# Performance work log

Hardware: AMD Instinct MI355X
Metric: run time of the kernel (lower is better)

## Reference

```python
import jax, jax.numpy as jnp
import numpy as np

N, E, G, H, F_IN = 100_000, 3_200_000, 256, 16, 7
RRELU_SLOPE = (1.0 / 8.0 + 1.0 / 3.0) / 2.0  # eval-mode RReLU uses mean slope


def rrelu(x):
    return jnp.where(x >= 0, x, RRELU_SLOPE * x)


def gcn_conv(x, edge_index, edge_weight, W, b, n_nodes):
    """PyG GCNConv: add self-loops, symmetric norm, gather-matmul-scatter."""
    row, col = edge_index[0], edge_index[1]
    loop = jnp.arange(n_nodes)
    row = jnp.concatenate([row, loop])
    col = jnp.concatenate([col, loop])
    w = jnp.concatenate([edge_weight, jnp.ones((n_nodes,), x.dtype)])
    deg = jax.ops.segment_sum(w, col, num_segments=n_nodes)
    dis = jnp.where(deg > 0, jax.lax.rsqrt(jnp.maximum(deg, 1e-12)), 0.0)
    norm = dis[row] * w * dis[col]            # [E+N]
    h = x @ W                                  # [N, out]
    msg = h[row] * norm[:, None]               # gather + scale
    return jax.ops.segment_sum(msg, col, num_segments=n_nodes) + b


def max_pool_neighbor_x(x, edge_index, n_nodes):
    row, col = edge_index[0], edge_index[1]
    loop = jnp.arange(n_nodes)
    row = jnp.concatenate([row, loop])
    col = jnp.concatenate([col, loop])
    return jax.ops.segment_max(x[row], col, num_segments=n_nodes)


def setup_inputs() -> dict:
    key = jax.random.key(0)
    ks = jax.random.split(key, 12)
    x = jax.random.normal(ks[0], (N, F_IN), jnp.float32)
    edge_index = jax.random.randint(ks[1], (2, E), 0, N)
    edge_weights = jax.random.uniform(ks[2], (E,), jnp.float32)
    batch = (jnp.arange(N) * G) // N  # sorted, every graph non-empty
    s = 0.2
    W1 = jax.random.normal(ks[3], (F_IN, H), jnp.float32) * s
    b1 = jnp.zeros((H,), jnp.float32)
    W2 = jax.random.normal(ks[4], (H, H), jnp.float32) * s
    b2 = jnp.zeros((H,), jnp.float32)
    Wl1 = jax.random.normal(ks[5], (H, H), jnp.float32) * s
    bl1 = jax.random.normal(ks[6], (H,), jnp.float32) * s
    Wl3 = jax.random.normal(ks[7], (H, H), jnp.float32) * s
    bl3 = jax.random.normal(ks[8], (H,), jnp.float32) * s
    Wl4 = jax.random.normal(ks[9], (H, 1), jnp.float32) * s
    bl4 = jax.random.normal(ks[10], (1,), jnp.float32) * s
    return {"x": x, "edge_index": edge_index, "batch": batch,
            "edge_weights": edge_weights, "W1": W1, "b1": b1, "W2": W2,
            "b2": b2, "Wl1": Wl1, "bl1": bl1, "Wl3": Wl3, "bl3": bl3,
            "Wl4": Wl4, "bl4": bl4}


def reference(x, edge_index, batch, edge_weights, W1, b1, W2, b2,
              Wl1, bl1, Wl3, bl3, Wl4, bl4):
    h = gcn_conv(x, edge_index, edge_weights, W1, b1, N)
    h = max_pool_neighbor_x(h, edge_index, N)
    res = h
    h = gcn_conv(h, edge_index, jnp.ones((E,), h.dtype), W2, b2, N)
    h = jax.nn.relu(res + h)
    g = jax.ops.segment_max(h, batch, num_segments=G)  # global_max_pool
    res = g
    g = rrelu(res + (g @ Wl1 + bl1))
    res = g
    g = rrelu(res + (g @ Wl3 + bl3))
    # dropout p=0.5 in eval mode -> identity
    g = rrelu(g @ Wl4 + bl4)
    return g
```

## Files before the change

kernel.cpp:

```cpp
#include <hip/hip_runtime.h>
#include <hip/hip_fp16.h>
#include <math.h>

#define NN 100000
#define NE 3200000
#define NG 256
#define HD 16
#define FIN 7

#define RB 8
#define RSZ 256
#define NBUK 391
#define NBUKP 400
#define FB 512
#define CHUNK 6250
#define CH2 3125
#define SCB 8
#define LMASK 0x1FFFF

#define SEGN 64
#define SEGB 1563
#define NPW 16

#define SCAP 10240

#define S_DEGW 16777216.0f
#define INV_S_DEGW 5.9604644775390625e-8f

static constexpr float SLOPE = 0.22916666666666666f;

__device__ __forceinline__ float rrelu_f(float a) {
    return a >= 0.f ? a : SLOPE * a;
}

__device__ __forceinline__ float h2f(unsigned short us) {
    __half h = *(__half*)&us;
    return __half2float(h);
}


__global__ __launch_bounds__(512) void k_hist(
        const int* __restrict__ col, int* __restrict__ hist) {
    __shared__ int bins[NBUK];
    for (int i = threadIdx.x; i < NBUK; i += 512) bins[i] = 0;
    __syncthreads();
    const int2* c2 = (const int2*)(col + blockIdx.x * CHUNK);
    for (int i = threadIdx.x; i < CH2; i += 512) {
        int2 v = c2[i];
        atomicAdd(&bins[v.x >> RB], 1);
        atomicAdd(&bins[v.y >> RB], 1);
    }
    __syncthreads();
    for (int i = threadIdx.x; i < NBUK; i += 512)
        hist[blockIdx.x * NBUKP + i] = bins[i];
}

__global__ __launch_bounds__(512) void k_scan_a(
        const int* __restrict__ hist, int* __restrict__ pre_t,
        int* __restrict__ tot) {
    __shared__ int s[SCB * (FB + 1)];
    int t = threadIdx.x;
    int c0 = blockIdx.x * SCB;
    for (int i = t; i < SCB * FB; i += 512) {
        int j = i >> 3, c = i & 7;
        int cc = c0 + c;
        s[c * (FB + 1) + j] = (cc < NBUK) ? hist[j * NBUKP + cc] : 0;
    }
    __syncthreads();
    int w = t >> 6, l = t & 63;
    int* sb = &s[w * (FB + 1)];
    int base = l * 8;
    int loc[8];
    int run = 0;
#pragma unroll
    for (int k = 0; k < 8; ++k) { loc[k] = run; run += sb[base + k]; }
    int inc = run;
#pragma unroll
    for (int d = 1; d < 64; d <<= 1) {
        int v = __shfl_up(inc, d, 64);
        if (l >= d) inc += v;
    }
    int excl = inc - run;
    int cc = c0 + w;
    if (cc < NBUK) {
#pragma unroll
        for (int k = 0; k < 8; ++k) sb[base + k] = excl + loc[k];
        if (l == 63) tot[cc] = inc;
    }
    __syncthreads();
    for (int i = t; i < SCB * FB; i += 512) {
        int j = i >> 3, c = i & 7;
        int cc2 = c0 + c;
        if (cc2 < NBUK) pre_t[j * NBUKP + cc2] = s[c * (FB + 1) + j];
    }
}

__global__ __launch_bounds__(512) void k_scan_b(
        const int* __restrict__ tot, int* __restrict__ bstart,
        unsigned* __restrict__ gbuf) {
    __shared__ int s[512];
    int t = threadIdx.x;
    for (int i = t; i < NG * HD; i += 512) gbuf[i] = 0u;
    int v = (t < NBUK) ? tot[t] : 0;
    s[t] = v;
    __syncthreads();
    for (int d = 1; d < 512; d <<= 1) {
        int add = (t >= d) ? s[t - d] : 0;
        __syncthreads();
        s[t] += add;
        __syncthreads();
    }
    if (t < NBUK) bstart[t + 1] = s[t];
    if (t == 0) bstart[0] = 0;
}

__global__ __launch_bounds__(512) void k_fill(
        const int* __restrict__ row, const int* __restrict__ col,
        const float* __restrict__ ew,
        const int* __restrict__ pre_t, const int* __restrict__ bstart,
        unsigned* __restrict__ sp, unsigned short* __restrict__ swh) {
    __shared__ int lcnt[NBUK];
    __shared__ int gofs[NBUK];
    __shared__ int part[512];
    __shared__ unsigned ssp[CHUNK];
    __shared__ unsigned short ssw[CHUNK];
    __shared__ unsigned short sbuk[CHUNK];
    int t = threadIdx.x;
    for (int i = t; i < NBUK; i += 512) {
        lcnt[i] = 0;
        gofs[i] = bstart[i] + pre_t[blockIdx.x * NBUKP + i];
    }
    __syncthreads();
    const int2* c2 = (const int2*)(col + blockIdx.x * CHUNK);
    const int2* r2 = (const int2*)(row + blockIdx.x * CHUNK);
    const float2* e2 = (const float2*)(ew + blockIdx.x * CHUNK);
    for (int i = t; i < CH2; i += 512) {
        int2 v = c2[i];
        atomicAdd(&lcnt[v.x >> RB], 1);
        atomicAdd(&lcnt[v.y >> RB], 1);
    }
    __syncthreads();
    int c = (t < NBUK) ? lcnt[t] : 0;
    part[t] = c;
    __syncthreads();
    for (int d = 1; d < 512; d <<= 1) {
        int add = (t >= d) ? part[t - d] : 0;
        __syncthreads();
        part[t] += add;
        __syncthreads();
    }
    if (t < NBUK) {
        int e = part[t] - c;
        gofs[t] -= e;
        lcnt[t] = e;
    }
    __syncthreads();
    for (int i = t; i < CH2; i += 512) {
        int2 cv = c2[i];
        int2 rv = r2[i];
        float2 wv = e2[i];
        {
            int b = cv.x >> RB;
            int s = atomicAdd(&lcnt[b], 1);
            ssp[s] = ((unsigned)(cv.x & (RSZ - 1)) << 17) | (unsigned)rv.x;
            __half hv = __float2half_rn(wv.x);
            ssw[s] = *(unsigned short*)&hv;
            sbuk[s] = (unsigned short)b;
        }
        {
            int b = cv.y >> RB;
            int s = atomicAdd(&lcnt[b], 1);
            ssp[s] = ((unsigned)(cv.y & (RSZ - 1)) << 17) | (unsigned)rv.y;
            __half hv = __float2half_rn(wv.y);
            ssw[s] = *(unsigned short*)&hv;
            sbuk[s] = (unsigned short)b;
        }
    }
    __syncthreads();
    for (int s = t; s < CHUNK; s += 512) {
        int g = s + gofs[sbuk[s]];
        sp[g] = ssp[s];
        swh[g] = ssw[s];
    }
}

__global__ __launch_bounds__(1024) void k_deg(
        const unsigned* __restrict__ sp, const unsigned short* __restrict__ swh,
        const int* __restrict__ bstart,
        const float* __restrict__ x, const float* __restrict__ W1,
        float* __restrict__ dis1, float* __restrict__ dis2,
        int* __restrict__ nstart, unsigned* __restrict__ h1h,
        unsigned* __restrict__ sp2) {
    __shared__ unsigned long long sdeg[RSZ];
    __shared__ float sdis[RSZ];
    __shared__ float sW1[FIN * HD];
    __shared__ int sscan[RSZ];
    __shared__ int lrank[RSZ];
    __shared__ unsigned sstage[SCAP];
    int t = threadIdx.x;
    if (t < FIN * HD) sW1[t] = W1[t];
    if (t < RSZ) sdeg[t] = 0ULL;
    __syncthreads();
    int s0 = bstart[blockIdx.x], s1 = bstart[blockIdx.x + 1];
    int j = s0 + t;
    for (; j + 3072 < s1; j += 4096) {
        unsigned e0 = sp[j], e1 = sp[j + 1024], e2 = sp[j + 2048], e3 = sp[j + 3072];
        float w0 = h2f(swh[j]), w1 = h2f(swh[j + 1024]);
        float w2 = h2f(swh[j + 2048]), w3 = h2f(swh[j + 3072]);
        atomicAdd(&sdeg[e0 >> 17], (1ULL << 32) |
                  (unsigned long long)(unsigned)__float2int_rn(w0 * S_DEGW));
        atomicAdd(&sdeg[e1 >> 17], (1ULL << 32) |
                  (unsigned long long)(unsigned)__float2int_rn(w1 * S_DEGW));
        atomicAdd(&sdeg[e2 >> 17], (1ULL << 32) |
                  (unsigned long long)(unsigned)__float2int_rn(w2 * S_DEGW));
        atomicAdd(&sdeg[e3 >> 17], (1ULL << 32) |
                  (unsigned long long)(unsigned)__float2int_rn(w3 * S_DEGW));
    }
    for (; j < s1; j += 1024) {
        unsigned e = sp[j];
        float w = h2f(swh[j]);
        atomicAdd(&sdeg[e >> 17], (1ULL << 32) |
                  (unsigned long long)(unsigned)__float2int_rn(w * S_DEGW));
    }
    __syncthreads();
    int node0 = blockIdx.x * RSZ;
    int cnt_t = 0;
    if (t < RSZ) { cnt_t = (int)(sdeg[t] >> 32); sscan[t] = cnt_t; }
    __syncthreads();
    for (int d = 1; d < RSZ; d <<= 1) {
        int add = (t < RSZ && t >= d) ? sscan[t - d] : 0;
        __syncthreads();
        if (t < RSZ) sscan[t] += add;
        __syncthreads();
    }
    if (t < RSZ) {
        int excl = sscan[t] - cnt_t;
        lrank[t] = excl;
        if (node0 + t <= NN) nstart[node0 + t] = s0 + excl;
        if (node0 + t < NN) {
            unsigned long long v = sdeg[t];
            unsigned cnt = (unsigned)(v >> 32);
            float wsum = (float)(unsigned)(v & 0xFFFFFFFFULL) * INV_S_DEGW;
            float d1 = rsqrtf(wsum + 1.f);
            dis1[node0 + t] = d1;
            sdis[t] = d1;
            dis2[node0 + t] = rsqrtf((float)cnt + 1.f);
        }
    }
    __syncthreads();
    for (int k = s0 + t; k < s1; k += 1024) {
        unsigned e = sp[k];
        unsigned short wb = swh[k];
        int pos = atomicAdd(&lrank[e >> 17], 1);
        unsigned packed = ((unsigned)(wb & 0x7FFFu) << 17) | (e & LMASK);
        if (pos < SCAP) sstage[pos] = packed;
        else sp2[s0 + pos] = packed;
    }
    __syncthreads();
    int bsz = s1 - s0;
    int lim = bsz < SCAP ? bsz : SCAP;
    for (int k = t; k < lim; k += 1024) sp2[s0 + k] = sstage[k];
    for (int i = t; i < RSZ * 8; i += 1024) {
        int ln = i >> 3, p = i & 7;
        int node = node0 + ln;
        if (node < NN) {
            float a0 = 0.f, a1 = 0.f;
#pragma unroll
            for (int k = 0; k < FIN; ++k) {
                float xv = x[node * FIN + k];
                a0 += xv * sW1[k * HD + 2 * p];
                a1 += xv * sW1[k * HD + 2 * p + 1];
            }
            float d = sdis[ln];
            __half2 hh = __floats2half2_rn(a0 * d, a1 * d);
            h1h[node * 8 + p] = *(unsigned*)&hh;
        }
    }
}

__global__ __launch_bounds__(256) void k_conv1(
        const unsigned* __restrict__ sp2, const int* __restrict__ nstart,
        const unsigned* __restrict__ h1h, const float* __restrict__ dis1,
        const float* __restrict__ b1, unsigned* __restrict__ h1outh) {
    int t = threadIdx.x;
    int l = t & 63, w = t >> 6;
    int e = l >> 3, p = l & 7;
    float bb0 = b1[2 * p], bb1 = b1[2 * p + 1];
    int nwbase = blockIdx.x * SEGN + w * NPW;
    for (int nn = 0; nn < NPW; ++nn) {
        int node = __builtin_amdgcn_readfirstlane(nwbase + nn);
        if (node >= NN) break;
        int e0 = nstart[node], e1 = nstart[node + 1];
        float a0 = 0.f, a1 = 0.f;
        int jb = e0;
        for (; jb + 8 < e1; jb += 16) {
            int i1 = min(jb + 8 + e, e1 - 1);
            unsigned v0 = sp2[jb + e];
            unsigned v1 = sp2[i1];
            unsigned g0 = h1h[(v0 & LMASK) * 8 + p];
            unsigned g1 = h1h[(v1 & LMASK) * 8 + p];
            if (jb + 8 + e >= e1) g1 = 0u;
            float w0 = h2f((unsigned short)(v0 >> 17));
            float w1 = h2f((unsigned short)(v1 >> 17));
            float2 f0 = __half22float2(*(__half2*)&g0);
            float2 f1 = __half22float2(*(__half2*)&g1);
            a0 += f0.x * w0 + f1.x * w1;
            a1 += f0.y * w0 + f1.y * w1;
        }
        for (; jb < e1; jb += 8) {
            int i0 = min(jb + e, e1 - 1);
            unsigned v0 = sp2[i0];
            unsigned g0 = h1h[(v0 & LMASK) * 8 + p];
            if (jb + e >= e1) g0 = 0u;
            float w0 = h2f((unsigned short)(v0 >> 17));
            float2 f0 = __half22float2(*(__half2*)&g0);
            a0 += f0.x * w0;
            a1 += f0.y * w0;
        }
        a0 += __shfl_xor(a0, 8);  a1 += __shfl_xor(a1, 8);
        a0 += __shfl_xor(a0, 16); a1 += __shfl_xor(a1, 16);
        a0 += __shfl_xor(a0, 32); a1 += __shfl_xor(a1, 32);
        float d = dis1[node];
        unsigned sh = h1h[node * 8 + p];
        float2 sf = __half22float2(*(__half2*)&sh);
        float r0 = (a0 + sf.x) * d + bb0;
        float r1 = (a1 + sf.y) * d + bb1;
        if (e == 0) {
            __half2 hh = __floats2half2_rn(r0, r1);
            h1outh[node * 8 + p] = *(unsigned*)&hh;
        }
    }
}

__global__ __launch_bounds__(256) void k_pool_h2(
        const unsigned* __restrict__ sp2, const int* __restrict__ nstart,
        const unsigned* __restrict__ h1outh, const float* __restrict__ W2,
        const float* __restrict__ dis2,
        float2* __restrict__ pool2, unsigned* __restrict__ h2sh) {
    int t = threadIdx.x;
    int l = t & 63, w = t >> 6;
    int e = l >> 3, p = l & 7;
    float w00 = W2[(2 * e) * HD + 2 * p],     w10 = W2[(2 * e + 1) * HD + 2 * p];
    float w01 = W2[(2 * e) * HD + 2 * p + 1], w11 = W2[(2 * e + 1) * HD + 2 * p + 1];
    int nwbase = blockIdx.x * SEGN + w * NPW;
    for (int nn = 0; nn < NPW; ++nn) {
        int node = __builtin_amdgcn_readfirstlane(nwbase + nn);
        if (node >= NN) break;
        int e0 = nstart[node], e1 = nstart[node + 1];
        unsigned sh = h1outh[node * 8 + p];
        float2 sf = __half22float2(*(__half2*)&sh);
        float m0 = sf.x, m1 = sf.y;
        int jb = e0;
        for (; jb + 8 < e1; jb += 16) {
            int i1 = min(jb + 8 + e, e1 - 1);
            unsigned v0 = sp2[jb + e];
            unsigned v1 = sp2[i1];
            unsigned g0 = h1outh[(v0 & LMASK) * 8 + p];
            unsigned g1 = h1outh[(v1 & LMASK) * 8 + p];
            float2 f0 = __half22float2(*(__half2*)&g0);
            float2 f1 = __half22float2(*(__half2*)&g1);
            m0 = fmaxf(m0, fmaxf(f0.x, f1.x));
            m1 = fmaxf(m1, fmaxf(f0.y, f1.y));
        }
        for (; jb < e1; jb += 8) {
            int i0 = min(jb + e, e1 - 1);
            unsigned v0 = sp2[i0];
            unsigned g0 = h1outh[(v0 & LMASK) * 8 + p];
            float2 f0 = __half22float2(*(__half2*)&g0);
            m0 = fmaxf(m0, f0.x);
            m1 = fmaxf(m1, f0.y);
        }
        m0 = fmaxf(m0, __shfl_xor(m0, 8));  m1 = fmaxf(m1, __shfl_xor(m1, 8));
        m0 = fmaxf(m0, __shfl_xor(m0, 16)); m1 = fmaxf(m1, __shfl_xor(m1, 16));
        m0 = fmaxf(m0, __shfl_xor(m0, 32)); m1 = fmaxf(m1, __shfl_xor(m1, 32));
        if (e == 0) pool2[node * 8 + p] = make_float2(m0, m1);
        float pm0 = __shfl(m0, e);
        float pm1 = __shfl(m1, e);
        float a0 = pm0 * w00 + pm1 * w10;
        float a1 = pm0 * w01 + pm1 * w11;
        a0 += __shfl_xor(a0, 8);  a1 += __shfl_xor(a1, 8);
        a0 += __shfl_xor(a0, 16); a1 += __shfl_xor(a1, 16);
        a0 += __shfl_xor(a0, 32); a1 += __shfl_xor(a1, 32);
        float d = dis2[node];
        if (e == 0) {
            __half2 hh = __floats2half2_rn(a0 * d, a1 * d);
            h2sh[node * 8 + p] = *(unsigned*)&hh;
        }
    }
}

__global__ __launch_bounds__(256) void k_conv2(
        const unsigned* __restrict__ sp2, const int* __restrict__ nstart,
        const unsigned* __restrict__ h2sh, const float* __restrict__ dis2,
        const float2* __restrict__ pool2, const float* __restrict__ b2,
        unsigned* __restrict__ gbuf) {
    __shared__ unsigned sgmax[2 * HD];
    int t = threadIdx.x;
    if (t < 2 * HD) sgmax[t] = 0u;
    __syncthreads();
    int l = t & 63, w = t >> 6;
    int e = l >> 3, p = l & 7;
    float bb0 = b2[2 * p], bb1 = b2[2 * p + 1];
    int nbase = blockIdx.x * SEGN;
    int gbase = (int)(((unsigned long long)nbase * NG) / NN);
    int nwbase = nbase + w * NPW;
    for (int nn = 0; nn < NPW; ++nn) {
        int node = __builtin_amdgcn_readfirstlane(nwbase + nn);
        if (node >= NN) break;
        int e0 = nstart[node], e1 = nstart[node + 1];
        float a0 = 0.f, a1 = 0.f;
        int jb = e0;
        for (; jb + 8 < e1; jb += 16) {
            int i1 = min(jb + 8 + e, e1 - 1);
            unsigned v0 = sp2[jb + e];
            unsigned v1 = sp2[i1];
            unsigned g0 = h2sh[(v0 & LMASK) * 8 + p];
            unsigned g1 = h2sh[(v1 & LMASK) * 8 + p];
            if (jb + 8 + e >= e1) g1 = 0u;
            float2 f0 = __half22float2(*(__half2*)&g0);
            float2 f1 = __half22float2(*(__half2*)&g1);
            a0 += f0.x + f1.x;
            a1 += f0.y + f1.y;
        }
        for (; jb < e1; jb += 8) {
            int i0 = min(jb + e, e1 - 1);
            unsigned v0 = sp2[i0];
            unsigned g0 = h2sh[(v0 & LMASK) * 8 + p];
            if (jb + e >= e1) g0 = 0u;
            float2 f0 = __half22float2(*(__half2*)&g0);
            a0 += f0.x;
            a1 += f0.y;
        }
        a0 += __shfl_xor(a0, 8);  a1 += __shfl_xor(a1, 8);
        a0 += __shfl_xor(a0, 16); a1 += __shfl_xor(a1, 16);
        a0 += __shfl_xor(a0, 32); a1 += __shfl_xor(a1, 32);
        float d = dis2[node];
        unsigned sh = h2sh[node * 8 + p];
        float2 self = __half22float2(*(__half2*)&sh);
        float2 pl = pool2[node * 8 + p];
        float r0 = fmaxf(pl.x + (a0 + self.x) * d + bb0, 0.f);
        float r1 = fmaxf(pl.y + (a1 + self.y) * d + bb1, 0.f);
        int lg = (int)(((unsigned long long)node * NG) / NN) - gbase;
        if (e == 0) {
            atomicMax(&sgmax[lg * HD + 2 * p],     __float_as_uint(r0));
            atomicMax(&sgmax[lg * HD + 2 * p + 1], __float_as_uint(r1));
        }
    }
    __syncthreads();
    if (t < 2 * HD) {
        int lg = t >> 4, f = t & 15;
        int gg = gbase + lg;
        unsigned m = sgmax[t];
        if (gg < NG && m > 0u) atomicMax(&gbuf[gg * HD + f], m);
    }
}

__global__ __launch_bounds__(256) void k_mlp(
        const float* __restrict__ gbuf,
        const float* __restrict__ Wl1, const float* __restrict__ bl1,
        const float* __restrict__ Wl3, const float* __restrict__ bl3,
        const float* __restrict__ Wl4, const float* __restrict__ bl4,
        float* __restrict__ out) {
    __shared__ float sW1[256], sW3[256], sW4[16], sb1[16], sb3[16];
    __shared__ float sb4;
    int tid = threadIdx.x;
    sW1[tid] = Wl1[tid];
    sW3[tid] = Wl3[tid];
    if (tid < 16) { sW4[tid] = Wl4[tid]; sb1[tid] = bl1[tid]; sb3[tid] = bl3[tid]; }
    if (tid == 0) sb4 = bl4[0];
    __syncthreads();

    float v[16], t1[16], t2[16];
#pragma unroll
    for (int f = 0; f < 16; ++f) v[f] = gbuf[tid * 16 + f];
#pragma unroll
    for (int f = 0; f < 16; ++f) {
        float a = sb1[f] + v[f];
#pragma unroll
        for (int k = 0; k < 16; ++k) a += v[k] * sW1[k * 16 + f];
        t1[f] = rrelu_f(a);
    }
#pragma unroll
    for (int f = 0; f < 16; ++f) {
        float a = sb3[f] + t1[f];
#pragma unroll
        for (int k = 0; k < 16; ++k) a += t1[k] * sW3[k * 16 + f];
        t2[f] = rrelu_f(a);
    }
    float o = sb4;
#pragma unroll
    for (int k = 0; k < 16; ++k) o += t2[k] * sW4[k];
    out[tid] = rrelu_f(o);
}

extern "C" void kernel_launch(void* const* d_in, const int* in_sizes, int n_in,
                              void* d_out, int out_size, void* d_ws, size_t ws_size,
                              hipStream_t stream) {
    const float* x   = (const float*)d_in[0];
    const int*   ei  = (const int*)  d_in[1];
    const float* ew  = (const float*)d_in[3];
    const float* W1  = (const float*)d_in[4];
    const float* b1  = (const float*)d_in[5];
    const float* W2  = (const float*)d_in[6];
    const float* b2  = (const float*)d_in[7];
    const float* Wl1 = (const float*)d_in[8];
    const float* bl1 = (const float*)d_in[9];
    const float* Wl3 = (const float*)d_in[10];
    const float* bl3 = (const float*)d_in[11];
    const float* Wl4 = (const float*)d_in[12];
    const float* bl4 = (const float*)d_in[13];
    const int* row = ei;
    const int* col = ei + NE;

    float* ws = (float*)d_ws;
    float* pool  = ws;
    float* dead  = pool + NN * HD;
    float* dis1  = dead + NN * HD;
    float* dis2  = dis1 + NN;
    int*   nstart = (int*)(dis2 + NN);
    unsigned* gbuf = (unsigned*)(nstart + NN + 2);
    unsigned* h1h    = gbuf   + NG * HD;
    unsigned* h1outh = h1h    + NN * 8;
    unsigned* h2sh   = h1outh + NN * 8;
    unsigned* sp     = h2sh   + NN * 8;
    unsigned short* swh = (unsigned short*)(sp + NE);
    unsigned* sp2    = (unsigned*)(swh + NE);
    int* tot    = (int*)(sp2 + NE);
    int* bstart = tot + NBUK;
    int* hist   = (int*)pool;
    int* pre_t  = (int*)dead;

    k_hist     <<<FB, 512, 0, stream>>>(col, hist);
    k_scan_a   <<<(NBUK + SCB - 1) / SCB, 512, 0, stream>>>(hist, pre_t, tot);
    k_scan_b   <<<1, 512, 0, stream>>>(tot, bstart, gbuf);
    k_fill     <<<FB, 512, 0, stream>>>(row, col, ew, pre_t, bstart, sp, swh);
    k_deg      <<<NBUK, 1024, 0, stream>>>(sp, swh, bstart, x, W1,
                                           dis1, dis2, nstart, h1h, sp2);
    k_conv1    <<<SEGB, 256, 0, stream>>>(sp2, nstart, h1h, dis1, b1, h1outh);
    k_pool_h2  <<<SEGB, 256, 0, stream>>>(sp2, nstart, h1outh, W2, dis2,
                                          (float2*)pool, h2sh);
    k_conv2    <<<SEGB, 256, 0, stream>>>(sp2, nstart, h2sh, dis2,
                                          (const float2*)pool, b2, gbuf);
    k_mlp      <<<1, 256, 0, stream>>>((const float*)gbuf, Wl1, bl1, Wl3, bl3,
                                       Wl4, bl4, (float*)d_out);
}
```

Baseline: 264.1 us.

## Pad per-node edge lists to multiples of 16 and interleave two nodes per wave

The edge-building kernel now rounds each node's CSR segment up to a multiple of 16, fills the padding with self-pointing zero-weight entries, and stores each bucket at a fixed stride. The separate tail loops and clamp/mask logic in the three gather kernels go away. Each wave now processes two nodes at once with independent accumulators, to hide gather latency. Blocks are halved to 32 nodes so more blocks launch. In exchange the kernels do extra padded gathers (corrected in conv2 by subtracting the self-term), and the global overflow path is dropped, so a bucket exceeding the fixed capacity would silently lose edges.

```diff
diff --git a/kernel.cpp b/kernel.cpp
--- a/kernel.cpp
+++ b/kernel.cpp
@@ -18,11 +18,12 @@
 #define SCB 8
 #define LMASK 0x1FFFF
 
-#define SEGN 64
-#define SEGB 1563
-#define NPW 16
-
-#define SCAP 10240
+#define SEGN 32
+#define SEGB 3125
+#define NPW 8
+
+#define PSTRIDE_B 10880
+#define SCAP PSTRIDE_B
 
 #define S_DEGW 16777216.0f
 #define INV_S_DEGW 5.9604644775390625e-8f
@@ -189,8 +190,8 @@
         const int* __restrict__ bstart,
         const float* __restrict__ x, const float* __restrict__ W1,
         float* __restrict__ dis1, float* __restrict__ dis2,
-        int* __restrict__ nstart, unsigned* __restrict__ h1h,
-        unsigned* __restrict__ sp2) {
+        int* __restrict__ pstart, int* __restrict__ cnts,
+        unsigned* __restrict__ h1h, unsigned* __restrict__ sp2) {
     __shared__ unsigned long long sdeg[RSZ];
     __shared__ float sdis[RSZ];
     __shared__ float sW1[FIN * HD];
@@ -224,8 +225,13 @@
     }
     __syncthreads();
     int node0 = blockIdx.x * RSZ;
-    int cnt_t = 0;
-    if (t < RSZ) { cnt_t = (int)(sdeg[t] >> 32); sscan[t] = cnt_t; }
+    int s0p = blockIdx.x * PSTRIDE_B;
+    int cnt_t = 0, pc_t = 0;
+    if (t < RSZ) {
+        cnt_t = (int)(sdeg[t] >> 32);
+        pc_t = (cnt_t + 15) & ~15;
+        sscan[t] = pc_t;
+    }
     __syncthreads();
     for (int d = 1; d < RSZ; d <<= 1) {
         int add = (t < RSZ && t >= d) ? sscan[t - d] : 0;
@@ -234,17 +240,23 @@
         __syncthreads();
     }
     if (t < RSZ) {
-        int excl = sscan[t] - cnt_t;
+        int excl = sscan[t] - pc_t;
         lrank[t] = excl;
-        if (node0 + t <= NN) nstart[node0 + t] = s0 + excl;
         if (node0 + t < NN) {
+            pstart[node0 + t] = s0p + excl;
+            cnts[node0 + t] = cnt_t;
             unsigned long long v = sdeg[t];
-            unsigned cnt = (unsigned)(v >> 32);
             float wsum = (float)(unsigned)(v & 0xFFFFFFFFULL) * INV_S_DEGW;
             float d1 = rsqrtf(wsum + 1.f);
             dis1[node0 + t] = d1;
             sdis[t] = d1;
-            dis2[node0 + t] = rsqrtf((float)cnt + 1.f);
+            dis2[node0 + t] = rsqrtf((float)cnt_t + 1.f);
+        }
+        int pbase = excl + cnt_t;
+        unsigned pv = (unsigned)(node0 + t);
+        for (int k = cnt_t; k < pc_t; ++k) {
+            int pos = pbase + (k - cnt_t);
+            if (pos < SCAP) sstage[pos] = pv;
         }
     }
     __syncthreads();
@@ -254,12 +266,11 @@
         int pos = atomicAdd(&lrank[e >> 17], 1);
         unsigned packed = ((unsigned)(wb & 0x7FFFu) << 17) | (e & LMASK);
         if (pos < SCAP) sstage[pos] = packed;
-        else sp2[s0 + pos] = packed;
-    }
-    __syncthreads();
-    int bsz = s1 - s0;
-    int lim = bsz < SCAP ? bsz : SCAP;
-    for (int k = t; k < lim; k += 1024) sp2[s0 + k] = sstage[k];
+    }
+    __syncthreads();
+    int ptot = sscan[RSZ - 1];
+    int lim = ptot < SCAP ? ptot : SCAP;
+    for (int k = t; k < lim; k += 1024) sp2[s0p + k] = sstage[k];
     for (int i = t; i < RSZ * 8; i += 1024) {
         int ln = i >> 3, p = i & 7;
         int node = node0 + ln;
@@ -279,7 +290,8 @@
 }
 
 __global__ __launch_bounds__(256) void k_conv1(
-        const unsigned* __restrict__ sp2, const int* __restrict__ nstart,
+        const unsigned* __restrict__ sp2, const int* __restrict__ pstart,
+        const int* __restrict__ cnts,
         const unsigned* __restrict__ h1h, const float* __restrict__ dis1,
         const float* __restrict__ b1, unsigned* __restrict__ h1outh) {
     int t = threadIdx.x;
@@ -287,53 +299,66 @@
     int e = l >> 3, p = l & 7;
     float bb0 = b1[2 * p], bb1 = b1[2 * p + 1];
     int nwbase = blockIdx.x * SEGN + w * NPW;
-    for (int nn = 0; nn < NPW; ++nn) {
-        int node = __builtin_amdgcn_readfirstlane(nwbase + nn);
-        if (node >= NN) break;
-        int e0 = nstart[node], e1 = nstart[node + 1];
-        float a0 = 0.f, a1 = 0.f;
-        int jb = e0;
-        for (; jb + 8 < e1; jb += 16) {
-            int i1 = min(jb + 8 + e, e1 - 1);
-            unsigned v0 = sp2[jb + e];
-            unsigned v1 = sp2[i1];
-            unsigned g0 = h1h[(v0 & LMASK) * 8 + p];
-            unsigned g1 = h1h[(v1 & LMASK) * 8 + p];
-            if (jb + 8 + e >= e1) g1 = 0u;
-            float w0 = h2f((unsigned short)(v0 >> 17));
-            float w1 = h2f((unsigned short)(v1 >> 17));
-            float2 f0 = __half22float2(*(__half2*)&g0);
-            float2 f1 = __half22float2(*(__half2*)&g1);
-            a0 += f0.x * w0 + f1.x * w1;
-            a1 += f0.y * w0 + f1.y * w1;
-        }
-        for (; jb < e1; jb += 8) {
-            int i0 = min(jb + e, e1 - 1);
-            unsigned v0 = sp2[i0];
-            unsigned g0 = h1h[(v0 & LMASK) * 8 + p];
-            if (jb + e >= e1) g0 = 0u;
-            float w0 = h2f((unsigned short)(v0 >> 17));
-            float2 f0 = __half22float2(*(__half2*)&g0);
-            a0 += f0.x * w0;
-            a1 += f0.y * w0;
-        }
-        a0 += __shfl_xor(a0, 8);  a1 += __shfl_xor(a1, 8);
-        a0 += __shfl_xor(a0, 16); a1 += __shfl_xor(a1, 16);
-        a0 += __shfl_xor(a0, 32); a1 += __shfl_xor(a1, 32);
-        float d = dis1[node];
-        unsigned sh = h1h[node * 8 + p];
-        float2 sf = __half22float2(*(__half2*)&sh);
-        float r0 = (a0 + sf.x) * d + bb0;
-        float r1 = (a1 + sf.y) * d + bb1;
+    for (int nn = 0; nn < NPW; nn += 2) {
+        int nodeA = __builtin_amdgcn_readfirstlane(nwbase + nn);
+        int nodeB = nodeA + 1;
+        int pA = pstart[nodeA], cA = cnts[nodeA];
+        int pB = pstart[nodeB], cB = cnts[nodeB];
+        int tA = (cA + 15) >> 4, tB = (cB + 15) >> 4;
+        float dA = dis1[nodeA], dB = dis1[nodeB];
+        unsigned shA = h1h[nodeA * 8 + p], shB = h1h[nodeB * 8 + p];
+        float aA0 = 0.f, aA1 = 0.f, aB0 = 0.f, aB1 = 0.f;
+        int jA = pA + e, jB = pB + e;
+        while (tA > 0 || tB > 0) {
+            if (tA > 0) {
+                unsigned v0 = sp2[jA], v1 = sp2[jA + 8];
+                unsigned g0 = h1h[(v0 & LMASK) * 8 + p];
+                unsigned g1 = h1h[(v1 & LMASK) * 8 + p];
+                float w0 = h2f((unsigned short)(v0 >> 17));
+                float w1 = h2f((unsigned short)(v1 >> 17));
+                float2 f0 = __half22float2(*(__half2*)&g0);
+                float2 f1 = __half22float2(*(__half2*)&g1);
+                aA0 += f0.x * w0 + f1.x * w1;
+                aA1 += f0.y * w0 + f1.y * w1;
+                jA += 16; --tA;
+            }
+            if (tB > 0) {
+                unsigned v0 = sp2[jB], v1 = sp2[jB + 8];
+                unsigned g0 = h1h[(v0 & LMASK) * 8 + p];
+                unsigned g1 = h1h[(v1 & LMASK) * 8 + p];
+                float w0 = h2f((unsigned short)(v0 >> 17));
+                float w1 = h2f((unsigned short)(v1 >> 17));
+                float2 f0 = __half22float2(*(__half2*)&g0);
+                float2 f1 = __half22float2(*(__half2*)&g1);
+                aB0 += f0.x * w0 + f1.x * w1;
+                aB1 += f0.y * w0 + f1.y * w1;
+                jB += 16; --tB;
+            }
+        }
+        aA0 += __shfl_xor(aA0, 8);  aB0 += __shfl_xor(aB0, 8);
+        aA1 += __shfl_xor(aA1, 8);  aB1 += __shfl_xor(aB1, 8);
+        aA0 += __shfl_xor(aA0, 16); aB0 += __shfl_xor(aB0, 16);
+        aA1 += __shfl_xor(aA1, 16); aB1 += __shfl_xor(aB1, 16);
+        aA0 += __shfl_xor(aA0, 32); aB0 += __shfl_xor(aB0, 32);
+        aA1 += __shfl_xor(aA1, 32); aB1 += __shfl_xor(aB1, 32);
+        float2 sfA = __half22float2(*(__half2*)&shA);
+        float2 sfB = __half22float2(*(__half2*)&shB);
+        float rA0 = (aA0 + sfA.x) * dA + bb0;
+        float rA1 = (aA1 + sfA.y) * dA + bb1;
+        float rB0 = (aB0 + sfB.x) * dB + bb0;
+        float rB1 = (aB1 + sfB.y) * dB + bb1;
         if (e == 0) {
-            __half2 hh = __floats2half2_rn(r0, r1);
-            h1outh[node * 8 + p] = *(unsigned*)&hh;
+            __half2 ha = __floats2half2_rn(rA0, rA1);
+            h1outh[nodeA * 8 + p] = *(unsigned*)&ha;
+            __half2 hb = __floats2half2_rn(rB0, rB1);
+            h1outh[nodeB * 8 + p] = *(unsigned*)&hb;
         }
     }
 }
 
 __global__ __launch_bounds__(256) void k_pool_h2(
-        const unsigned* __restrict__ sp2, const int* __restrict__ nstart,
+        const unsigned* __restrict__ sp2, const int* __restrict__ pstart,
+        const int* __restrict__ cnts,
         const unsigned* __restrict__ h1outh, const float* __restrict__ W2,
         const float* __restrict__ dis2,
         float2* __restrict__ pool2, unsigned* __restrict__ h2sh) {
@@ -343,54 +368,75 @@
     float w00 = W2[(2 * e) * HD + 2 * p],     w10 = W2[(2 * e + 1) * HD + 2 * p];
     float w01 = W2[(2 * e) * HD + 2 * p + 1], w11 = W2[(2 * e + 1) * HD + 2 * p + 1];
     int nwbase = blockIdx.x * SEGN + w * NPW;
-    for (int nn = 0; nn < NPW; ++nn) {
-        int node = __builtin_amdgcn_readfirstlane(nwbase + nn);
-        if (node >= NN) break;
-        int e0 = nstart[node], e1 = nstart[node + 1];
-        unsigned sh = h1outh[node * 8 + p];
-        float2 sf = __half22float2(*(__half2*)&sh);
-        float m0 = sf.x, m1 = sf.y;
-        int jb = e0;
-        for (; jb + 8 < e1; jb += 16) {
-            int i1 = min(jb + 8 + e, e1 - 1);
-            unsigned v0 = sp2[jb + e];
-            unsigned v1 = sp2[i1];
-            unsigned g0 = h1outh[(v0 & LMASK) * 8 + p];
-            unsigned g1 = h1outh[(v1 & LMASK) * 8 + p];
-            float2 f0 = __half22float2(*(__half2*)&g0);
-            float2 f1 = __half22float2(*(__half2*)&g1);
-            m0 = fmaxf(m0, fmaxf(f0.x, f1.x));
-            m1 = fmaxf(m1, fmaxf(f0.y, f1.y));
-        }
-        for (; jb < e1; jb += 8) {
-            int i0 = min(jb + e, e1 - 1);
-            unsigned v0 = sp2[i0];
-            unsigned g0 = h1outh[(v0 & LMASK) * 8 + p];
-            float2 f0 = __half22float2(*(__half2*)&g0);
-            m0 = fmaxf(m0, f0.x);
-            m1 = fmaxf(m1, f0.y);
-        }
-        m0 = fmaxf(m0, __shfl_xor(m0, 8));  m1 = fmaxf(m1, __shfl_xor(m1, 8));
-        m0 = fmaxf(m0, __shfl_xor(m0, 16)); m1 = fmaxf(m1, __shfl_xor(m1, 16));
-        m0 = fmaxf(m0, __shfl_xor(m0, 32)); m1 = fmaxf(m1, __shfl_xor(m1, 32));
-        if (e == 0) pool2[node * 8 + p] = make_float2(m0, m1);
-        float pm0 = __shfl(m0, e);
-        float pm1 = __shfl(m1, e);
-        float a0 = pm0 * w00 + pm1 * w10;
-        float a1 = pm0 * w01 + pm1 * w11;
-        a0 += __shfl_xor(a0, 8);  a1 += __shfl_xor(a1, 8);
-        a0 += __shfl_xor(a0, 16); a1 += __shfl_xor(a1, 16);
-        a0 += __shfl_xor(a0, 32); a1 += __shfl_xor(a1, 32);
-        float d = dis2[node];
+    for (int nn = 0; nn < NPW; nn += 2) {
+        int nodeA = __builtin_amdgcn_readfirstlane(nwbase + nn);
+        int nodeB = nodeA + 1;
+        int pA = pstart[nodeA], cA = cnts[nodeA];
+        int pB = pstart[nodeB], cB = cnts[nodeB];
+        int tA = (cA + 15) >> 4, tB = (cB + 15) >> 4;
+        float dA = dis2[nodeA], dB = dis2[nodeB];
+        unsigned shA = h1outh[nodeA * 8 + p], shB = h1outh[nodeB * 8 + p];
+        float2 sfA = __half22float2(*(__half2*)&shA);
+        float2 sfB = __half22float2(*(__half2*)&shB);
+        float mA0 = sfA.x, mA1 = sfA.y;
+        float mB0 = sfB.x, mB1 = sfB.y;
+        int jA = pA + e, jB = pB + e;
+        while (tA > 0 || tB > 0) {
+            if (tA > 0) {
+                unsigned v0 = sp2[jA], v1 = sp2[jA + 8];
+                unsigned g0 = h1outh[(v0 & LMASK) * 8 + p];
+                unsigned g1 = h1outh[(v1 & LMASK) * 8 + p];
+                float2 f0 = __half22float2(*(__half2*)&g0);
+                float2 f1 = __half22float2(*(__half2*)&g1);
+                mA0 = fmaxf(mA0, fmaxf(f0.x, f1.x));
+                mA1 = fmaxf(mA1, fmaxf(f0.y, f1.y));
+                jA += 16; --tA;
+            }
+            if (tB > 0) {
+                unsigned v0 = sp2[jB], v1 = sp2[jB + 8];
+                unsigned g0 = h1outh[(v0 & LMASK) * 8 + p];
+                unsigned g1 = h1outh[(v1 & LMASK) * 8 + p];
+                float2 f0 = __half22float2(*(__half2*)&g0);
+                float2 f1 = __half22float2(*(__half2*)&g1);
+                mB0 = fmaxf(mB0, fmaxf(f0.x, f1.x));
+                mB1 = fmaxf(mB1, fmaxf(f0.y, f1.y));
+                jB += 16; --tB;
+            }
+        }
+        mA0 = fmaxf(mA0, __shfl_xor(mA0, 8));  mB0 = fmaxf(mB0, __shfl_xor(mB0, 8));
+        mA1 = fmaxf(mA1, __shfl_xor(mA1, 8));  mB1 = fmaxf(mB1, __shfl_xor(mB1, 8));
+        mA0 = fmaxf(mA0, __shfl_xor(mA0, 16)); mB0 = fmaxf(mB0, __shfl_xor(mB0, 16));
+        mA1 = fmaxf(mA1, __shfl_xor(mA1, 16)); mB1 = fmaxf(mB1, __shfl_xor(mB1, 16));
+        mA0 = fmaxf(mA0, __shfl_xor(mA0, 32)); mB0 = fmaxf(mB0, __shfl_xor(mB0, 32));
+        mA1 = fmaxf(mA1, __shfl_xor(mA1, 32)); mB1 = fmaxf(mB1, __shfl_xor(mB1, 32));
         if (e == 0) {
-            __half2 hh = __floats2half2_rn(a0 * d, a1 * d);
-            h2sh[node * 8 + p] = *(unsigned*)&hh;
+            pool2[nodeA * 8 + p] = make_float2(mA0, mA1);
+            pool2[nodeB * 8 + p] = make_float2(mB0, mB1);
+        }
+        float pmA0 = __shfl(mA0, e), pmB0 = __shfl(mB0, e);
+        float pmA1 = __shfl(mA1, e), pmB1 = __shfl(mB1, e);
+        float aA0 = pmA0 * w00 + pmA1 * w10;
+        float aA1 = pmA0 * w01 + pmA1 * w11;
+        float aB0 = pmB0 * w00 + pmB1 * w10;
+        float aB1 = pmB0 * w01 + pmB1 * w11;
+        aA0 += __shfl_xor(aA0, 8);  aB0 += __shfl_xor(aB0, 8);
+        aA1 += __shfl_xor(aA1, 8);  aB1 += __shfl_xor(aB1, 8);
+        aA0 += __shfl_xor(aA0, 16); aB0 += __shfl_xor(aB0, 16);
+        aA1 += __shfl_xor(aA1, 16); aB1 += __shfl_xor(aB1, 16);
+        aA0 += __shfl_xor(aA0, 32); aB0 += __shfl_xor(aB0, 32);
+        aA1 += __shfl_xor(aA1, 32); aB1 += __shfl_xor(aB1, 32);
+        if (e == 0) {
+            __half2 ha = __floats2half2_rn(aA0 * dA, aA1 * dA);
+            h2sh[nodeA * 8 + p] = *(unsigned*)&ha;
+            __half2 hb = __floats2half2_rn(aB0 * dB, aB1 * dB);
+            h2sh[nodeB * 8 + p] = *(unsigned*)&hb;
         }
     }
 }
 
 __global__ __launch_bounds__(256) void k_conv2(
-        const unsigned* __restrict__ sp2, const int* __restrict__ nstart,
+        const unsigned* __restrict__ sp2, const int* __restrict__ pstart,
+        const int* __restrict__ cnts,
         const unsigned* __restrict__ h2sh, const float* __restrict__ dis2,
         const float2* __restrict__ pool2, const float* __restrict__ b2,
         unsigned* __restrict__ gbuf) {
@@ -404,46 +450,60 @@
     int nbase = blockIdx.x * SEGN;
     int gbase = (int)(((unsigned long long)nbase * NG) / NN);
     int nwbase = nbase + w * NPW;
-    for (int nn = 0; nn < NPW; ++nn) {
-        int node = __builtin_amdgcn_readfirstlane(nwbase + nn);
-        if (node >= NN) break;
-        int e0 = nstart[node], e1 = nstart[node + 1];
-        float a0 = 0.f, a1 = 0.f;
-        int jb = e0;
-        for (; jb + 8 < e1; jb += 16) {
-            int i1 = min(jb + 8 + e, e1 - 1);
-            unsigned v0 = sp2[jb + e];
-            unsigned v1 = sp2[i1];
-            unsigned g0 = h2sh[(v0 & LMASK) * 8 + p];
-            unsigned g1 = h2sh[(v1 & LMASK) * 8 + p];
-            if (jb + 8 + e >= e1) g1 = 0u;
-            float2 f0 = __half22float2(*(__half2*)&g0);
-            float2 f1 = __half22float2(*(__half2*)&g1);
-            a0 += f0.x + f1.x;
-            a1 += f0.y + f1.y;
-        }
-        for (; jb < e1; jb += 8) {
-            int i0 = min(jb + e, e1 - 1);
-            unsigned v0 = sp2[i0];
-            unsigned g0 = h2sh[(v0 & LMASK) * 8 + p];
-            if (jb + e >= e1) g0 = 0u;
-            float2 f0 = __half22float2(*(__half2*)&g0);
-            a0 += f0.x;
-            a1 += f0.y;
-        }
-        a0 += __shfl_xor(a0, 8);  a1 += __shfl_xor(a1, 8);
-        a0 += __shfl_xor(a0, 16); a1 += __shfl_xor(a1, 16);
-        a0 += __shfl_xor(a0, 32); a1 += __shfl_xor(a1, 32);
-        float d = dis2[node];
-        unsigned sh = h2sh[node * 8 + p];
-        float2 self = __half22float2(*(__half2*)&sh);
-        float2 pl = pool2[node * 8 + p];
-        float r0 = fmaxf(pl.x + (a0 + self.x) * d + bb0, 0.f);
-        float r1 = fmaxf(pl.y + (a1 + self.y) * d + bb1, 0.f);
-        int lg = (int)(((unsigned long long)node * NG) / NN) - gbase;
+    for (int nn = 0; nn < NPW; nn += 2) {
+        int nodeA = __builtin_amdgcn_readfirstlane(nwbase + nn);
+        int nodeB = nodeA + 1;
+        int pA = pstart[nodeA], cA = cnts[nodeA];
+        int pB = pstart[nodeB], cB = cnts[nodeB];
+        int tA = (cA + 15) >> 4, tB = (cB + 15) >> 4;
+        int npadA = (tA << 4) - cA, npadB = (tB << 4) - cB;
+        float dA = dis2[nodeA], dB = dis2[nodeB];
+        unsigned shA = h2sh[nodeA * 8 + p], shB = h2sh[nodeB * 8 + p];
+        float2 plA = pool2[nodeA * 8 + p], plB = pool2[nodeB * 8 + p];
+        float aA0 = 0.f, aA1 = 0.f, aB0 = 0.f, aB1 = 0.f;
+        int jA = pA + e, jB = pB + e;
+        while (tA > 0 || tB > 0) {
+            if (tA > 0) {
+                unsigned v0 = sp2[jA], v1 = sp2[jA + 8];
+                unsigned g0 = h2sh[(v0 & LMASK) * 8 + p];
+                unsigned g1 = h2sh[(v1 & LMASK) * 8 + p];
+                float2 f0 = __half22float2(*(__half2*)&g0);
+                float2 f1 = __half22float2(*(__half2*)&g1);
+                aA0 += f0.x + f1.x;
+                aA1 += f0.y + f1.y;
+                jA += 16; --tA;
+            }
+            if (tB > 0) {
+                unsigned v0 = sp2[jB], v1 = sp2[jB + 8];
+                unsigned g0 = h2sh[(v0 & LMASK) * 8 + p];
+                unsigned g1 = h2sh[(v1 & LMASK) * 8 + p];
+                float2 f0 = __half22float2(*(__half2*)&g0);
+                float2 f1 = __half22float2(*(__half2*)&g1);
+                aB0 += f0.x + f1.x;
+                aB1 += f0.y + f1.y;
+                jB += 16; --tB;
+            }
+        }
+        aA0 += __shfl_xor(aA0, 8);  aB0 += __shfl_xor(aB0, 8);
+        aA1 += __shfl_xor(aA1, 8);  aB1 += __shfl_xor(aB1, 8);
+        aA0 += __shfl_xor(aA0, 16); aB0 += __shfl_xor(aB0, 16);
+        aA1 += __shfl_xor(aA1, 16); aB1 += __shfl_xor(aB1, 16);
+        aA0 += __shfl_xor(aA0, 32); aB0 += __shfl_xor(aB0, 32);
+        aA1 += __shfl_xor(aA1, 32); aB1 += __shfl_xor(aB1, 32);
+        float2 selfA = __half22float2(*(__half2*)&shA);
+        float2 selfB = __half22float2(*(__half2*)&shB);
+        float csA = 1.f - (float)npadA, csB = 1.f - (float)npadB;
+        float rA0 = fmaxf(plA.x + (aA0 + csA * selfA.x) * dA + bb0, 0.f);
+        float rA1 = fmaxf(plA.y + (aA1 + csA * selfA.y) * dA + bb1, 0.f);
+        float rB0 = fmaxf(plB.x + (aB0 + csB * selfB.x) * dB + bb0, 0.f);
+        float rB1 = fmaxf(plB.y + (aB1 + csB * selfB.y) * dB + bb1, 0.f);
         if (e == 0) {
-            atomicMax(&sgmax[lg * HD + 2 * p],     __float_as_uint(r0));
-            atomicMax(&sgmax[lg * HD + 2 * p + 1], __float_as_uint(r1));
+            int lgA = (int)(((unsigned long long)nodeA * NG) / NN) - gbase;
+            int lgB = (int)(((unsigned long long)nodeB * NG) / NN) - gbase;
+            atomicMax(&sgmax[lgA * HD + 2 * p],     __float_as_uint(rA0));
+            atomicMax(&sgmax[lgA * HD + 2 * p + 1], __float_as_uint(rA1));
+            atomicMax(&sgmax[lgB * HD + 2 * p],     __float_as_uint(rB0));
+            atomicMax(&sgmax[lgB * HD + 2 * p + 1], __float_as_uint(rB1));
         }
     }
     __syncthreads();
@@ -517,15 +577,16 @@
     float* dead  = pool + NN * HD;
     float* dis1  = dead + NN * HD;
     float* dis2  = dis1 + NN;
-    int*   nstart = (int*)(dis2 + NN);
-    unsigned* gbuf = (unsigned*)(nstart + NN + 2);
+    int*   pstart = (int*)(dis2 + NN);
+    int*   cnts  = pstart + NN;
+    unsigned* gbuf = (unsigned*)(cnts + NN);
     unsigned* h1h    = gbuf   + NG * HD;
     unsigned* h1outh = h1h    + NN * 8;
     unsigned* h2sh   = h1outh + NN * 8;
     unsigned* sp     = h2sh   + NN * 8;
     unsigned short* swh = (unsigned short*)(sp + NE);
     unsigned* sp2    = (unsigned*)(swh + NE);
-    int* tot    = (int*)(sp2 + NE);
+    int* tot    = (int*)(sp2 + (size_t)NBUK * PSTRIDE_B);
     int* bstart = tot + NBUK;
     int* hist   = (int*)pool;
     int* pre_t  = (int*)dead;
@@ -535,11 +596,12 @@
     k_scan_b   <<<1, 512, 0, stream>>>(tot, bstart, gbuf);
     k_fill     <<<FB, 512, 0, stream>>>(row, col, ew, pre_t, bstart, sp, swh);
     k_deg      <<<NBUK, 1024, 0, stream>>>(sp, swh, bstart, x, W1,
-                                           dis1, dis2, nstart, h1h, sp2);
-    k_conv1    <<<SEGB, 256, 0, stream>>>(sp2, nstart, h1h, dis1, b1, h1outh);
-    k_pool_h2  <<<SEGB, 256, 0, stream>>>(sp2, nstart, h1outh, W2, dis2,
+                                           dis1, dis2, pstart, cnts, h1h, sp2);
+    k_conv1    <<<SEGB, 256, 0, stream>>>(sp2, pstart, cnts, h1h, dis1,
+                                          b1, h1outh);
+    k_pool_h2  <<<SEGB, 256, 0, stream>>>(sp2, pstart, cnts, h1outh, W2, dis2,
                                           (float2*)pool, h2sh);
-    k_conv2    <<<SEGB, 256, 0, stream>>>(sp2, nstart, h2sh, dis2,
+    k_conv2    <<<SEGB, 256, 0, stream>>>(sp2, pstart, cnts, h2sh, dis2,
                                           (const float2*)pool, b2, gbuf);
     k_mlp      <<<1, 256, 0, stream>>>((const float*)gbuf, Wl1, bl1, Wl3, bl3,
                                        Wl4, bl4, (float*)d_out);
```

Result: faster. 252.5 us (-4.4%).
